# Performance work log

Hardware: AMD Instinct MI355X
Metric: run time of the kernel (lower is better)

Reference implementation:

```python
import jax, jax.numpy as jnp
import numpy as np


def _axial_mha(x, Wq, Wk, Wv, Wo, bo, n_head, axis):
    # x: (B, T, H, W, C) channels-last video features
    B, T, H, W, C = x.shape
    d = C // n_head
    scale = 1.0 / np.sqrt(d)

    def proj(w):
        return (x @ w.T).reshape(B, T, H, W, n_head, d)

    q, k, v = proj(Wq), proj(Wk), proj(Wv)
    if axis == 'w':  # attend along width
        s = jnp.einsum('bthwnd,bthvnd->bthnwv', q, k) * scale
        a = jax.nn.softmax(s, axis=-1)
        o = jnp.einsum('bthnwv,bthvnd->bthwnd', a, v)
    elif axis == 'h':  # attend along height
        s = jnp.einsum('bthwnd,btgwnd->btwnhg', q, k) * scale
        a = jax.nn.softmax(s, axis=-1)
        o = jnp.einsum('btwnhg,btgwnd->bthwnd', a, v)
    else:  # 't' attend along time
        s = jnp.einsum('bthwnd,bshwnd->bhwnts', q, k) * scale
        a = jax.nn.softmax(s, axis=-1)
        o = jnp.einsum('bhwnts,bshwnd->bthwnd', a, v)
    o = o.reshape(B, T, H, W, C)
    return o @ Wo.T + bo


def setup_inputs() -> dict:
    key = jax.random.key(0)
    ks = jax.random.split(key, 16)
    B, C, T, H, W = 4, 512, 16, 32, 32
    std = 1.0 / np.sqrt(C)
    inp = {'x': jax.random.normal(ks[0], (B, C, T, H, W), jnp.float32)}
    i = 1
    for ax in ('w', 'h', 't'):
        for nm in ('wq', 'wk', 'wv', 'wo'):
            inp[f'{nm}_{ax}'] = jax.random.normal(ks[i], (C, C), jnp.float32) * std
            i += 1
        inp[f'bo_{ax}'] = jnp.zeros((C,), jnp.float32)
    inp['n_head'] = 8
    return inp


def reference(x, wq_w, wk_w, wv_w, wo_w, bo_w,
              wq_h, wk_h, wv_h, wo_h, bo_h,
              wq_t, wk_t, wv_t, wo_t, bo_t, n_head):
    xt = jnp.moveaxis(x, 1, -1)  # (B, T, H, W, C)
    out = (_axial_mha(xt, wq_w, wk_w, wv_w, wo_w, bo_w, n_head, 'w')
           + _axial_mha(xt, wq_h, wk_h, wv_h, wo_h, bo_h, n_head, 'h')
           + _axial_mha(xt, wq_t, wk_t, wv_t, wo_t, bo_t, n_head, 't'))
    return jnp.moveaxis(out, -1, 1)  # (B, C, T, H, W)
```

## Files before the change

### kernel.cpp

```cpp
#include <hip/hip_runtime.h>

typedef float f4 __attribute__((ext_vector_type(4)));
typedef int i4 __attribute__((ext_vector_type(4)));
typedef __bf16 bf16x8 __attribute__((ext_vector_type(8)));
typedef unsigned short u16;

#define DEV static __device__ __forceinline__

DEV f4 mfma_bf16(bf16x8 a, bf16x8 b, f4 c) {
  return __builtin_amdgcn_mfma_f32_16x16x32_bf16(a, b, c, 0, 0, 0);
}

DEV bf16x8 ld_frag(const u16* p) {
  union { i4 i; bf16x8 b; } u;
  u.i = *(const i4*)p;
  return u.b;
}

DEV u16 f2bf(float f) {
  union { float f; unsigned int u; } v; v.f = f;
  return (u16)((v.u + 0x7fffu + ((v.u >> 16) & 1u)) >> 16);
}

DEV void async_cp16(const void* g, void* l) {
  __builtin_amdgcn_global_load_lds((const __attribute__((address_space(1))) void*)g,
                                   (__attribute__((address_space(3))) void*)l, 16, 0, 0);
}

__global__ __launch_bounds__(256) void k_transpose_x(const float* __restrict__ x,
                                                     u16* __restrict__ xt) {
  __shared__ float tile[32][33];
  const int b = blockIdx.z;
  const int thw0 = blockIdx.x * 32;
  const int c0 = blockIdx.y * 32;
  const int tc = threadIdx.x & 31;
  const int tr = threadIdx.x >> 5;
#pragma unroll
  for (int i = 0; i < 4; i++) {
    int c = tr + i * 8;
    tile[c][tc] = x[(long)(b * 512 + c0 + c) * 16384 + thw0 + tc];
  }
  __syncthreads();
#pragma unroll
  for (int i = 0; i < 4; i++) {
    int r = tr + i * 8;
    xt[(long)(b * 16384 + thw0 + r) * 512 + c0 + tc] = f2bf(tile[tc][r]);
  }
}

__global__ __launch_bounds__(256) void k_prep_w(
    const float* wq_w, const float* wk_w, const float* wv_w, const float* wo_w, const float* bo_w,
    const float* wq_h, const float* wk_h, const float* wv_h, const float* wo_h, const float* bo_h,
    const float* wq_t, const float* wk_t, const float* wv_t, const float* wo_t, const float* bo_t,
    u16* Wqkv, u16* WoCat, float* bo) {
  const int idx = blockIdx.x * 256 + threadIdx.x;
  if (idx < 2359296) {
    int j = idx >> 9, ci = idx & 511;
    int sel = j >> 9, co = j & 511;
    const float* s;
    switch (sel) {
      case 0: s = wq_w; break; case 1: s = wk_w; break; case 2: s = wv_w; break;
      case 3: s = wq_h; break; case 4: s = wk_h; break; case 5: s = wv_h; break;
      case 6: s = wq_t; break; case 7: s = wk_t; break; default: s = wv_t; break;
    }
    Wqkv[idx] = f2bf(s[co * 512 + ci]);
  } else if (idx < 2359296 + 786432) {
    int t = idx - 2359296;
    int c = t / 1536, j2 = t - c * 1536;
    int a = j2 >> 9, ci = j2 & 511;
    const float* s = (a == 0) ? wo_w : (a == 1) ? wo_h : wo_t;
    WoCat[t] = f2bf(s[c * 512 + ci]);
  } else if (idx < 2359296 + 786432 + 512) {
    int c = idx - (2359296 + 786432);
    bo[c] = bo_w[c] + bo_h[c] + bo_t[c];
  }
}

__global__ __launch_bounds__(256, 2) void k_gemm_bt(
    const u16* __restrict__ A, const u16* __restrict__ Bt, u16* __restrict__ Co,
    int K, int lda, int ldb, int ldc) {
  __shared__ __attribute__((aligned(16))) u16 lds[20480];
  u16* ldsA = lds;
  u16* ldsB = lds + 8192;
  const int tid = threadIdx.x;
  const int lane = tid & 63, wave = tid >> 6;
  const int cl = lane & 15, q = lane >> 4;
  const int wm = (wave >> 1) * 64, wn = (wave & 1) * 64;
  const long m0 = (long)blockIdx.y * 128;
  const long n0 = (long)blockIdx.x * 128;
  const u16* Ab = A + m0 * lda;
  const u16* Bb = Bt + n0 * ldb;

  long a_off[4], b_off[4];
  u16 *a_dst[4], *b_dst[4];
#pragma unroll
  for (int i = 0; i < 4; i++) {
    int s = i * 256 + tid;
    int row = s >> 3;
    int gc = (s & 7) ^ (row & 7);
    a_off[i] = (long)row * lda + gc * 8;
    b_off[i] = (long)row * ldb + gc * 8;
    int slot0 = i * 256 + (tid & 192);
    a_dst[i] = ldsA + slot0 * 8;
    b_dst[i] = ldsB + slot0 * 8;
  }

  f4 acc[4][4];
  {
    f4 z; z[0] = z[1] = z[2] = z[3] = 0.f;
#pragma unroll
    for (int i = 0; i < 4; i++)
#pragma unroll
      for (int j = 0; j < 4; j++) acc[i][j] = z;
  }

  for (int kt = 0; kt < K; kt += 64) {
#pragma unroll
    for (int i = 0; i < 4; i++) {
      async_cp16(Ab + a_off[i] + kt, a_dst[i]);
      async_cp16(Bb + b_off[i] + kt, b_dst[i]);
    }
    __syncthreads();
#pragma unroll
    for (int kk = 0; kk < 2; kk++) {
      bf16x8 afr[4], bfr[4];
#pragma unroll
      for (int im = 0; im < 4; im++) {
        int row = wm + im * 16 + cl;
        int ch = (kk * 4 + q) ^ (row & 7);
        afr[im] = ld_frag(ldsA + row * 64 + ch * 8);
      }
#pragma unroll
      for (int in = 0; in < 4; in++) {
        int row = wn + in * 16 + cl;
        int ch = (kk * 4 + q) ^ (row & 7);
        bfr[in] = ld_frag(ldsB + row * 64 + ch * 8);
      }
#pragma unroll
      for (int im = 0; im < 4; im++)
#pragma unroll
        for (int in = 0; in < 4; in++)
          acc[im][in] = mfma_bf16(afr[im], bfr[in], acc[im][in]);
    }
    __syncthreads();
  }

  u16* myl = lds + wave * 5120;
#pragma unroll
  for (int im = 0; im < 4; im++)
#pragma unroll
    for (int in = 0; in < 4; in++)
#pragma unroll
      for (int r = 0; r < 4; r++)
        myl[(im * 16 + q * 4 + r) * 80 + in * 16 + cl] = f2bf(acc[im][in][r]);
  __syncthreads();
#pragma unroll
  for (int it = 0; it < 8; it++) {
    int lr = it * 8 + (lane >> 3);
    int lc = (lane & 7) * 8;
    i4 v = *(const i4*)(myl + lr * 80 + lc);
    *(i4*)(Co + (m0 + wm + lr) * ldc + n0 + wn + lc) = v;
  }
}

__global__ __launch_bounds__(1024, 4) void k_gemm_final(
    const u16* __restrict__ A, const u16* __restrict__ Bt,
    float* __restrict__ Co, const float* __restrict__ bias) {
  __shared__ __attribute__((aligned(16))) u16 lds[32768];
  u16* ldsA = lds;
  u16* ldsB = lds + 16384;
  const int tid = threadIdx.x;
  const int lane = tid & 63, wave = tid >> 6;
  const int cl = lane & 15, q = lane >> 4;
  const int wm = (wave >> 2) * 64, wn = (wave & 3) * 64;
  const int m0 = blockIdx.y * 256;
  const long n0 = (long)blockIdx.x * 256;
  const u16* Ab = A + (long)m0 * 1536;
  const u16* Bb = Bt + n0 * 1536;

  long a_off[2];
  u16 *a_dst[2], *b_dst[2];
#pragma unroll
  for (int i = 0; i < 2; i++) {
    int s = i * 1024 + tid;
    int row = s >> 3;
    int gc = (s & 7) ^ (row & 7);
    a_off[i] = (long)row * 1536 + gc * 8;
    int slot0 = i * 1024 + (tid & 960);
    a_dst[i] = ldsA + slot0 * 8;
    b_dst[i] = ldsB + slot0 * 8;
  }

  f4 acc[4][4];
  {
    f4 z; z[0] = z[1] = z[2] = z[3] = 0.f;
#pragma unroll
    for (int i = 0; i < 4; i++)
#pragma unroll
      for (int j = 0; j < 4; j++) acc[i][j] = z;
  }

  for (int kt = 0; kt < 1536; kt += 64) {
#pragma unroll
    for (int i = 0; i < 2; i++) {
      async_cp16(Ab + a_off[i] + kt, a_dst[i]);
      async_cp16(Bb + a_off[i] + kt, b_dst[i]);
    }
    __syncthreads();
#pragma unroll
    for (int kk = 0; kk < 2; kk++) {
      bf16x8 afr[4], bfr[4];
#pragma unroll
      for (int im = 0; im < 4; im++) {
        int row = wm + im * 16 + cl;
        int ch = (kk * 4 + q) ^ (row & 7);
        afr[im] = ld_frag(ldsA + row * 64 + ch * 8);
      }
#pragma unroll
      for (int in = 0; in < 4; in++) {
        int row = wn + in * 16 + cl;
        int ch = (kk * 4 + q) ^ (row & 7);
        bfr[in] = ld_frag(ldsB + row * 64 + ch * 8);
      }
#pragma unroll
      for (int im = 0; im < 4; im++)
#pragma unroll
        for (int in = 0; in < 4; in++)
          acc[im][in] = mfma_bf16(afr[im], bfr[in], acc[im][in]);
    }
    __syncthreads();
  }

#pragma unroll
  for (int im = 0; im < 4; im++)
#pragma unroll
    for (int r = 0; r < 4; r++) {
      int c = m0 + wm + im * 16 + q * 4 + r;
      float bv = bias[c];
#pragma unroll
      for (int in = 0; in < 4; in++) {
        long n = n0 + wn + in * 16 + cl;
        long b = n >> 14, thw = n & 16383;
        Co[((b * 512 + c) << 14) + thw] = acc[im][in][r] + bv;
      }
    }
}

template <int L>
__global__ __launch_bounds__(64) void k_attn(
    const u16* __restrict__ QKV, u16* __restrict__ Oc,
    int inner, int istride, int ostride, int obase, int tstride) {
  constexpr int NT = L / 16;
  __shared__ __attribute__((aligned(16))) u16 sQ[2048];
  __shared__ __attribute__((aligned(16))) u16 sK[2048];
  __shared__ __attribute__((aligned(16))) u16 sVt[2560];
  __shared__ __attribute__((aligned(16))) u16 sPbuf[(L == 16) ? 1280 : 1];
  u16* sP = (L == 16) ? sPbuf : sQ;
  const int lane = threadIdx.x;
  const int cl = lane & 15, q = lane >> 4;
  const int g = blockIdx.x, head = blockIdx.y;
  const long tok0 = (long)(g / inner) * ostride + (long)(g % inner) * istride;
  const long rs = (long)tstride * 1536;
  const u16* qb = QKV + tok0 * 1536 + head * 64;
  const u16* kb = qb + 512;
  const u16* vb = qb + 1024;

  if (L == 16) {
    unsigned int* z1 = (unsigned int*)sVt;
    for (int i = lane; i < 1280; i += 64) z1[i] = 0;
    unsigned int* z2 = (unsigned int*)sPbuf;
    for (int i = lane; i < 640; i += 64) z2[i] = 0;
  }

#pragma unroll
  for (int i = 0; i < L / 8; i++) {
    int s = i * 64 + lane;
    int row = s >> 3;
    int gc = (s & 7) ^ (row & 7);
    async_cp16(qb + row * rs + gc * 8, (char*)sQ + i * 1024);
    async_cp16(kb + row * rs + gc * 8, (char*)sK + i * 1024);
  }
#pragma unroll
  for (int i = 0; i < L / 8; i++) {
    int s = i * 64 + lane;
    int row = s >> 3, c8 = s & 7;
    union { i4 v; u16 h[8]; } raw;
    raw.v = *(const i4*)(vb + row * rs + c8 * 8);
#pragma unroll
    for (int j = 0; j < 8; j++) sVt[(c8 * 8 + j) * 40 + row] = raw.h[j];
  }
  __syncthreads();

  f4 sacc[NT][NT];
  { f4 z; z[0]=z[1]=z[2]=z[3]=0.f;
    for (int a = 0; a < NT; a++) for (int b2 = 0; b2 < NT; b2++) sacc[a][b2] = z; }
#pragma unroll
  for (int kk = 0; kk < 2; kk++) {
    bf16x8 qf[NT], kf[NT];
#pragma unroll
    for (int t = 0; t < NT; t++) {
      int row = t * 16 + cl;
      int ch = (kk * 4 + q) ^ (row & 7);
      qf[t] = ld_frag(sQ + row * 64 + ch * 8);
      kf[t] = ld_frag(sK + row * 64 + ch * 8);
    }
#pragma unroll
    for (int rt = 0; rt < NT; rt++)
#pragma unroll
      for (int ct = 0; ct < NT; ct++)
        sacc[rt][ct] = mfma_bf16(qf[rt], kf[ct], sacc[rt][ct]);
  }

#pragma unroll
  for (int rt = 0; rt < NT; rt++)
#pragma unroll
    for (int ct = 0; ct < NT; ct++)
#pragma unroll
      for (int i = 0; i < 4; i++) sacc[rt][ct][i] *= 0.125f;
#pragma unroll
  for (int rt = 0; rt < NT; rt++)
#pragma unroll
    for (int i = 0; i < 4; i++) {
      float m = sacc[rt][0][i];
#pragma unroll
      for (int ct = 1; ct < NT; ct++) m = fmaxf(m, sacc[rt][ct][i]);
      for (int off = 1; off < 16; off <<= 1) m = fmaxf(m, __shfl_xor(m, off, 64));
      float ssum = 0.f;
#pragma unroll
      for (int ct = 0; ct < NT; ct++) {
        float p = __expf(sacc[rt][ct][i] - m);
        sacc[rt][ct][i] = p;
        ssum += p;
      }
      for (int off = 1; off < 16; off <<= 1) ssum += __shfl_xor(ssum, off, 64);
      float inv = 1.0f / ssum;
#pragma unroll
      for (int ct = 0; ct < NT; ct++) sacc[rt][ct][i] *= inv;
    }

#pragma unroll
  for (int rt = 0; rt < NT; rt++)
#pragma unroll
    for (int ct = 0; ct < NT; ct++)
#pragma unroll
      for (int i = 0; i < 4; i++)
        sP[(rt * 16 + q * 4 + i) * 40 + ct * 16 + cl] = f2bf(sacc[rt][ct][i]);
  __syncthreads();

  bf16x8 pf[NT], vf[4];
#pragma unroll
  for (int mt = 0; mt < NT; mt++) pf[mt] = ld_frag(sP + (mt * 16 + cl) * 40 + q * 8);
#pragma unroll
  for (int nt = 0; nt < 4; nt++) vf[nt] = ld_frag(sVt + (nt * 16 + cl) * 40 + q * 8);
  f4 oacc[NT][4];
  { f4 z; z[0]=z[1]=z[2]=z[3]=0.f;
    for (int a = 0; a < NT; a++) for (int b2 = 0; b2 < 4; b2++) oacc[a][b2] = z; }
#pragma unroll
  for (int mt = 0; mt < NT; mt++)
#pragma unroll
    for (int nt = 0; nt < 4; nt++)
      oacc[mt][nt] = mfma_bf16(pf[mt], vf[nt], oacc[mt][nt]);

#pragma unroll
  for (int mt = 0; mt < NT; mt++)
#pragma unroll
    for (int i = 0; i < 4; i++) {
      int r = mt * 16 + q * 4 + i;
      u16* dst = Oc + (tok0 + (long)r * tstride) * 1536 + obase + head * 64;
#pragma unroll
      for (int nt = 0; nt < 4; nt++) dst[nt * 16 + cl] = f2bf(oacc[mt][nt][i]);
    }
}

extern "C" void kernel_launch(void* const* d_in, const int* in_sizes, int n_in,
                              void* d_out, int out_size, void* d_ws, size_t ws_size,
                              hipStream_t stream) {
  (void)in_sizes; (void)n_in; (void)out_size; (void)ws_size;
  const float* x    = (const float*)d_in[0];
  const float* wq_w = (const float*)d_in[1];
  const float* wk_w = (const float*)d_in[2];
  const float* wv_w = (const float*)d_in[3];
  const float* wo_w = (const float*)d_in[4];
  const float* bo_w = (const float*)d_in[5];
  const float* wq_h = (const float*)d_in[6];
  const float* wk_h = (const float*)d_in[7];
  const float* wv_h = (const float*)d_in[8];
  const float* wo_h = (const float*)d_in[9];
  const float* bo_h = (const float*)d_in[10];
  const float* wq_t = (const float*)d_in[11];
  const float* wk_t = (const float*)d_in[12];
  const float* wv_t = (const float*)d_in[13];
  const float* wo_t = (const float*)d_in[14];
  const float* bo_t = (const float*)d_in[15];

  char* ws = (char*)d_ws;
  u16* xt    = (u16*)(ws);
  u16* qkv   = (u16*)(ws + 67108864L);
  u16* oc    = (u16*)(ws + 268435456L);
  u16* Wqkv  = (u16*)(ws + 469762048L);
  u16* WoCat = (u16*)(ws + 474480640L);
  float* bo  = (float*)(ws + 476053504L);

  k_transpose_x<<<dim3(512, 16, 4), 256, 0, stream>>>(x, xt);
  k_prep_w<<<dim3(12290), 256, 0, stream>>>(wq_w, wk_w, wv_w, wo_w, bo_w,
                                            wq_h, wk_h, wv_h, wo_h, bo_h,
                                            wq_t, wk_t, wv_t, wo_t, bo_t,
                                            Wqkv, WoCat, bo);
  for (int a = 0; a < 3; a++) {
    k_gemm_bt<<<dim3(12, 512), 256, 0, stream>>>(
        xt, Wqkv + (long)a * 1536 * 512, qkv, 512, 512, 512, 1536);
    if (a == 0)
      k_attn<32><<<dim3(2048, 8), 64, 0, stream>>>(qkv, oc, 1, 0, 32, 0, 1);
    else if (a == 1)
      k_attn<32><<<dim3(2048, 8), 64, 0, stream>>>(qkv, oc, 32, 1, 1024, 512, 32);
    else
      k_attn<16><<<dim3(4096, 8), 64, 0, stream>>>(qkv, oc, 1024, 1, 16384, 1024, 1024);
  }
  k_gemm_final<<<dim3(256, 2), 1024, 0, stream>>>(WoCat, oc, (float*)d_out, bo);
}
```

Before: 961.3 us.

## Unify GEMMs into 256x256 tiled kernel with 4-stage async LDS pipeline

Replaces the separate QKV and output-projection GEMM kernels with one templated 256x256-tile kernel using 8 waves. It keeps a 4-buffer async global-to-LDS pipeline with partial vmcnt waits instead of a full sync every K step. It also adds grouped block-index swizzling for L2 locality, raised wave priority around the MFMA runs, and a new LDS swizzle. The cost is 128KB of LDS per block and more accumulator registers, which may limit occupancy.

```diff
diff --git a/kernel.cpp b/kernel.cpp
--- a/kernel.cpp
+++ b/kernel.cpp
@@ -76,174 +76,152 @@
   }
 }
 
-__global__ __launch_bounds__(256, 2) void k_gemm_bt(
-    const u16* __restrict__ A, const u16* __restrict__ Bt, u16* __restrict__ Co,
-    int K, int lda, int ldb, int ldc) {
-  __shared__ __attribute__((aligned(16))) u16 lds[20480];
+template <int NK, int EPI, int NT, int MT, bool MMINOR>
+__global__ __launch_bounds__(512, 2) void k_gemm256(
+    const u16* __restrict__ A, const u16* __restrict__ Bt,
+    void* __restrict__ Co, const float* __restrict__ bias, int ldc) {
+  constexpr int K = NK * 32;
+  __shared__ __attribute__((aligned(16))) u16 lds[65536];
   u16* ldsA = lds;
-  u16* ldsB = lds + 8192;
+  u16* ldsB = lds + 32768;
+
   const int tid = threadIdx.x;
   const int lane = tid & 63, wave = tid >> 6;
   const int cl = lane & 15, q = lane >> 4;
-  const int wm = (wave >> 1) * 64, wn = (wave & 1) * 64;
-  const long m0 = (long)blockIdx.y * 128;
-  const long n0 = (long)blockIdx.x * 128;
-  const u16* Ab = A + m0 * lda;
-  const u16* Bb = Bt + n0 * ldb;
-
-  long a_off[4], b_off[4];
-  u16 *a_dst[4], *b_dst[4];
-#pragma unroll
-  for (int i = 0; i < 4; i++) {
-    int s = i * 256 + tid;
-    int row = s >> 3;
-    int gc = (s & 7) ^ (row & 7);
-    a_off[i] = (long)row * lda + gc * 8;
-    b_off[i] = (long)row * ldb + gc * 8;
-    int slot0 = i * 256 + (tid & 192);
-    a_dst[i] = ldsA + slot0 * 8;
-    b_dst[i] = ldsB + slot0 * 8;
-  }
-
-  f4 acc[4][4];
+  const int wr = wave >> 2, wc = wave & 3;
+
+  const int bid = blockIdx.x;
+  const int orig = (bid & 7) * ((NT * MT) >> 3) + (bid >> 3);
+  const int my = MMINOR ? (orig % MT) : (orig / NT);
+  const int nx = MMINOR ? (orig / MT) : (orig % NT);
+  const long m0 = (long)my * 256;
+  const long n0 = (long)nx * 256;
+  const u16* Ab = A + m0 * K;
+  const u16* Bb = Bt + n0 * K;
+
+  long g_off[2];
+  int dslot[2];
+#pragma unroll
+  for (int i = 0; i < 2; i++) {
+    int s = i * 512 + tid;
+    int row = s >> 2;
+    int g = ((s & 3) - (row >> 2)) & 3;
+    g_off[i] = (long)row * K + g * 8;
+    dslot[i] = (i * 512 + (tid & 448)) * 8;
+  }
+
+  f4 acc[8][4];
   {
     f4 z; z[0] = z[1] = z[2] = z[3] = 0.f;
 #pragma unroll
-    for (int i = 0; i < 4; i++)
-#pragma unroll
-      for (int j = 0; j < 4; j++) acc[i][j] = z;
-  }
-
-  for (int kt = 0; kt < K; kt += 64) {
-#pragma unroll
-    for (int i = 0; i < 4; i++) {
-      async_cp16(Ab + a_off[i] + kt, a_dst[i]);
-      async_cp16(Bb + b_off[i] + kt, b_dst[i]);
-    }
+    for (int m = 0; m < 8; m++)
+#pragma unroll
+      for (int n = 0; n < 4; n++) acc[m][n] = z;
+  }
+
+#pragma unroll
+  for (int t = 0; t < 3; t++) {
+#pragma unroll
+    for (int i = 0; i < 2; i++) {
+      async_cp16(Ab + g_off[i] + t * 32, ldsA + t * 8192 + dslot[i]);
+      async_cp16(Bb + g_off[i] + t * 32, ldsB + t * 8192 + dslot[i]);
+    }
+  }
+  asm volatile("s_waitcnt vmcnt(8)\n\ts_barrier" ::: "memory");
+
+  const int ch = ((q + (cl >> 2)) & 3) * 8;
+  const int rowA = (wr * 128 + cl) * 32 + ch;
+  const int rowB = (wc * 64 + cl) * 32 + ch;
+
+  const u16* pa0 = Ab + g_off[0] + 96;
+  const u16* pa1 = Ab + g_off[1] + 96;
+  const u16* pb0 = Bb + g_off[0] + 96;
+  const u16* pb1 = Bb + g_off[1] + 96;
+
+#define STAGE(sb)                                              \
+  {                                                            \
+    async_cp16(pa0, ldsA + (sb) * 8192 + dslot[0]);            \
+    async_cp16(pb0, ldsB + (sb) * 8192 + dslot[0]);            \
+    async_cp16(pa1, ldsA + (sb) * 8192 + dslot[1]);            \
+    async_cp16(pb1, ldsB + (sb) * 8192 + dslot[1]);            \
+    pa0 += 32; pa1 += 32; pb0 += 32; pb1 += 32;                \
+  }
+
+#define COMPUTE(buf)                                           \
+  {                                                            \
+    const u16* bA = ldsA + (buf) * 8192;                       \
+    const u16* bB = ldsB + (buf) * 8192;                       \
+    bf16x8 af[8], bfr[4];                                      \
+    _Pragma("unroll")                                          \
+    for (int m = 0; m < 8; m++) af[m] = ld_frag(bA + rowA + m * 512);  \
+    _Pragma("unroll")                                          \
+    for (int n = 0; n < 4; n++) bfr[n] = ld_frag(bB + rowB + n * 512); \
+    __builtin_amdgcn_s_setprio(1);                             \
+    _Pragma("unroll")                                          \
+    for (int m = 0; m < 8; m++)                                \
+      _Pragma("unroll")                                        \
+      for (int n = 0; n < 4; n++)                              \
+        acc[m][n] = mfma_bf16(af[m], bfr[n], acc[m][n]);       \
+    __builtin_amdgcn_s_setprio(0);                             \
+  }
+
+  for (int tt = 0; tt < NK - 4; tt += 4) {
+#pragma unroll
+    for (int u = 0; u < 4; u++) {
+      STAGE((u + 3) & 3);
+      COMPUTE(u);
+      asm volatile("s_waitcnt vmcnt(8)\n\ts_barrier" ::: "memory");
+    }
+  }
+  STAGE(3);
+  COMPUTE(0);
+  asm volatile("s_waitcnt vmcnt(8)\n\ts_barrier" ::: "memory");
+  COMPUTE(1);
+  asm volatile("s_waitcnt vmcnt(4)\n\ts_barrier" ::: "memory");
+  COMPUTE(2);
+  asm volatile("s_waitcnt vmcnt(0)\n\ts_barrier" ::: "memory");
+  COMPUTE(3);
+#undef STAGE
+#undef COMPUTE
+
+  if (EPI == 0) {
     __syncthreads();
-#pragma unroll
-    for (int kk = 0; kk < 2; kk++) {
-      bf16x8 afr[4], bfr[4];
-#pragma unroll
-      for (int im = 0; im < 4; im++) {
-        int row = wm + im * 16 + cl;
-        int ch = (kk * 4 + q) ^ (row & 7);
-        afr[im] = ld_frag(ldsA + row * 64 + ch * 8);
+    u16* myl = lds + wave * 4608;
+    u16* CoB = (u16*)Co;
+#pragma unroll
+    for (int h = 0; h < 2; h++) {
+      if (h) __syncthreads();
+#pragma unroll
+      for (int m = 0; m < 4; m++)
+#pragma unroll
+        for (int n = 0; n < 4; n++)
+#pragma unroll
+          for (int r = 0; r < 4; r++)
+            myl[(m * 16 + q * 4 + r) * 72 + n * 16 + cl] = f2bf(acc[h * 4 + m][n][r]);
+#pragma unroll
+      for (int it = 0; it < 8; it++) {
+        int lr = it * 8 + (lane >> 3);
+        int lc = (lane & 7) * 8;
+        i4 v = *(const i4*)(myl + lr * 72 + lc);
+        *(i4*)(CoB + (m0 + wr * 128 + h * 64 + lr) * ldc + n0 + wc * 64 + lc) = v;
       }
-#pragma unroll
-      for (int in = 0; in < 4; in++) {
-        int row = wn + in * 16 + cl;
-        int ch = (kk * 4 + q) ^ (row & 7);
-        bfr[in] = ld_frag(ldsB + row * 64 + ch * 8);
+    }
+  } else {
+    float* Cf = (float*)Co;
+#pragma unroll
+    for (int m = 0; m < 8; m++)
+#pragma unroll
+      for (int r = 0; r < 4; r++) {
+        int c = (int)m0 + wr * 128 + m * 16 + q * 4 + r;
+        float bv = bias[c];
+#pragma unroll
+        for (int n = 0; n < 4; n++) {
+          long nn = n0 + wc * 64 + n * 16 + cl;
+          long b = nn >> 14, thw = nn & 16383;
+          Cf[((b * 512 + c) << 14) + thw] = acc[m][n][r] + bv;
+        }
       }
-#pragma unroll
-      for (int im = 0; im < 4; im++)
-#pragma unroll
-        for (int in = 0; in < 4; in++)
-          acc[im][in] = mfma_bf16(afr[im], bfr[in], acc[im][in]);
-    }
-    __syncthreads();
-  }
-
-  u16* myl = lds + wave * 5120;
-#pragma unroll
-  for (int im = 0; im < 4; im++)
-#pragma unroll
-    for (int in = 0; in < 4; in++)
-#pragma unroll
-      for (int r = 0; r < 4; r++)
-        myl[(im * 16 + q * 4 + r) * 80 + in * 16 + cl] = f2bf(acc[im][in][r]);
-  __syncthreads();
-#pragma unroll
-  for (int it = 0; it < 8; it++) {
-    int lr = it * 8 + (lane >> 3);
-    int lc = (lane & 7) * 8;
-    i4 v = *(const i4*)(myl + lr * 80 + lc);
-    *(i4*)(Co + (m0 + wm + lr) * ldc + n0 + wn + lc) = v;
-  }
-}
-
-__global__ __launch_bounds__(1024, 4) void k_gemm_final(
-    const u16* __restrict__ A, const u16* __restrict__ Bt,
-    float* __restrict__ Co, const float* __restrict__ bias) {
-  __shared__ __attribute__((aligned(16))) u16 lds[32768];
-  u16* ldsA = lds;
-  u16* ldsB = lds + 16384;
-  const int tid = threadIdx.x;
-  const int lane = tid & 63, wave = tid >> 6;
-  const int cl = lane & 15, q = lane >> 4;
-  const int wm = (wave >> 2) * 64, wn = (wave & 3) * 64;
-  const int m0 = blockIdx.y * 256;
-  const long n0 = (long)blockIdx.x * 256;
-  const u16* Ab = A + (long)m0 * 1536;
-  const u16* Bb = Bt + n0 * 1536;
-
-  long a_off[2];
-  u16 *a_dst[2], *b_dst[2];
-#pragma unroll
-  for (int i = 0; i < 2; i++) {
-    int s = i * 1024 + tid;
-    int row = s >> 3;
-    int gc = (s & 7) ^ (row & 7);
-    a_off[i] = (long)row * 1536 + gc * 8;
-    int slot0 = i * 1024 + (tid & 960);
-    a_dst[i] = ldsA + slot0 * 8;
-    b_dst[i] = ldsB + slot0 * 8;
-  }
-
-  f4 acc[4][4];
-  {
-    f4 z; z[0] = z[1] = z[2] = z[3] = 0.f;
-#pragma unroll
-    for (int i = 0; i < 4; i++)
-#pragma unroll
-      for (int j = 0; j < 4; j++) acc[i][j] = z;
-  }
-
-  for (int kt = 0; kt < 1536; kt += 64) {
-#pragma unroll
-    for (int i = 0; i < 2; i++) {
-      async_cp16(Ab + a_off[i] + kt, a_dst[i]);
-      async_cp16(Bb + a_off[i] + kt, b_dst[i]);
-    }
-    __syncthreads();
-#pragma unroll
-    for (int kk = 0; kk < 2; kk++) {
-      bf16x8 afr[4], bfr[4];
-#pragma unroll
-      for (int im = 0; im < 4; im++) {
-        int row = wm + im * 16 + cl;
-        int ch = (kk * 4 + q) ^ (row & 7);
-        afr[im] = ld_frag(ldsA + row * 64 + ch * 8);
-      }
-#pragma unroll
-      for (int in = 0; in < 4; in++) {
-        int row = wn + in * 16 + cl;
-        int ch = (kk * 4 + q) ^ (row & 7);
-        bfr[in] = ld_frag(ldsB + row * 64 + ch * 8);
-      }
-#pragma unroll
-      for (int im = 0; im < 4; im++)
-#pragma unroll
-        for (int in = 0; in < 4; in++)
-          acc[im][in] = mfma_bf16(afr[im], bfr[in], acc[im][in]);
-    }
-    __syncthreads();
-  }
-
-#pragma unroll
-  for (int im = 0; im < 4; im++)
-#pragma unroll
-    for (int r = 0; r < 4; r++) {
-      int c = m0 + wm + im * 16 + q * 4 + r;
-      float bv = bias[c];
-#pragma unroll
-      for (int in = 0; in < 4; in++) {
-        long n = n0 + wn + in * 16 + cl;
-        long b = n >> 14, thw = n & 16383;
-        Co[((b * 512 + c) << 14) + thw] = acc[im][in][r] + bv;
-      }
-    }
+  }
 }
 
 template <int L>
@@ -407,8 +385,8 @@
                                             wq_t, wk_t, wv_t, wo_t, bo_t,
                                             Wqkv, WoCat, bo);
   for (int a = 0; a < 3; a++) {
-    k_gemm_bt<<<dim3(12, 512), 256, 0, stream>>>(
-        xt, Wqkv + (long)a * 1536 * 512, qkv, 512, 512, 512, 1536);
+    k_gemm256<16, 0, 6, 256, false><<<dim3(1536), 512, 0, stream>>>(
+        xt, Wqkv + (long)a * 1536 * 512, qkv, nullptr, 1536);
     if (a == 0)
       k_attn<32><<<dim3(2048, 8), 64, 0, stream>>>(qkv, oc, 1, 0, 32, 0, 1);
     else if (a == 1)
@@ -416,5 +394,6 @@
     else
       k_attn<16><<<dim3(4096, 8), 64, 0, stream>>>(qkv, oc, 1024, 1, 16384, 1024, 1024);
   }
-  k_gemm_final<<<dim3(256, 2), 1024, 0, stream>>>(WoCat, oc, (float*)d_out, bo);
-}
+  k_gemm256<48, 1, 256, 2, true><<<dim3(512), 512, 0, stream>>>(
+      WoCat, oc, (float*)d_out, bo, 0);
+}
```

New measurement: 961.8 us. Within noise of the previous version (+0.1%).
